# Kernel optimization log

Hardware: AMD Instinct MI355X
Metric: run time of the kernel (lower is better)

Reference implementation:

```python
import jax, jax.numpy as jnp
import numpy as np

N, E, H, R = 20000, 400000, 128, 20


def setup_inputs() -> dict:
    key = jax.random.key(0)
    ks = jax.random.split(key, 12)
    inv_h = 1.0 / np.sqrt(H)
    inv_r = 1.0 / np.sqrt(R)
    return {
        "s": jax.random.normal(ks[0], (N, H), jnp.float32),
        "v": jax.random.normal(ks[1], (N, 3, H), jnp.float32),
        "edge_rbf": jax.random.normal(ks[2], (E, R), jnp.float32),
        "edge_cutoff": jax.random.uniform(ks[3], (E,), jnp.float32),
        "edge_vec": jax.random.normal(ks[4], (E, 3), jnp.float32),
        "W1": jax.random.normal(ks[5], (H, H), jnp.float32) * inv_h,
        "b1": jnp.zeros((H,), jnp.float32),
        "W2": jax.random.normal(ks[6], (H, 3 * H), jnp.float32) * inv_h,
        "b2": jnp.zeros((3 * H,), jnp.float32),
        "Wr": jax.random.normal(ks[7], (R, 3 * H), jnp.float32) * inv_r,
        "br": jnp.zeros((3 * H,), jnp.float32),
        "edge_index": jax.random.randint(ks[8], (2, E), 0, N, jnp.int64),
    }


def reference(s, v, edge_rbf, edge_cutoff, edge_vec, W1, b1, W2, b2, Wr, br, edge_index):
    i, j = edge_index[0], edge_index[1]
    n = s.shape[0]
    # rbf projection modulated by cutoff: [E, 3H]
    W = (edge_rbf @ Wr + br) * edge_cutoff[:, None]
    # scalar MLP on gathered source features: [E, 3H]
    h = jax.nn.silu(s[j] @ W1 + b1)
    x = (h @ W2 + b2) * W
    x_ss, x_sv, x_vv = jnp.split(x, 3, axis=-1)  # each [E, H]
    ds = jax.ops.segment_sum(x_ss, i, num_segments=n)
    # dv1: outer product of edge direction with gated scalars -> [E,3,H]
    dv1 = jax.ops.segment_sum(x_sv[:, None, :] * edge_vec[:, :, None], i, num_segments=n)
    # equivariant term: project v_j onto edge direction, re-expand
    inner = jnp.sum(v[j] * edge_vec[:, :, None], axis=1)  # [E, H]
    dv2 = jax.ops.segment_sum((inner * x_vv)[:, None, :] * edge_vec[:, :, None], i, num_segments=n)
    return ds, dv1 + dv2
```

## Files before the change

kernel.cpp:

```cpp
#include <hip/hip_runtime.h>
#include <hip/hip_bf16.h>

#define HDIM 128
#define H3   384
#define RDIM 20
#define NPB  16
#define NPR  4
#define CHNK 16

typedef unsigned short u16;
typedef unsigned int   u32;
typedef __attribute__((ext_vector_type(8))) short short8v;
typedef __attribute__((ext_vector_type(4))) float f32x4;

__device__ __forceinline__ u16 f2bf(float f) {
    __hip_bfloat16 h = __float2bfloat16(f);
    return *(u16*)&h;
}
__device__ __forceinline__ float bf2f(u16 u) {
    union { u32 i; float f; } x; x.i = (u32)u << 16; return x.f;
}
__device__ __forceinline__ float bflo(u32 u) {
    union { u32 i; float f; } x; x.i = u << 16; return x.f;
}
__device__ __forceinline__ float bfhi(u32 u) {
    union { u32 i; float f; } x; x.i = u & 0xffff0000u; return x.f;
}
__device__ __forceinline__ u32 pk(float lo, float hi) {
    return (u32)f2bf(lo) | ((u32)f2bf(hi) << 16);
}

__global__ __launch_bounds__(128) void node_mlp_kernel(
    const float* __restrict__ s, const float* __restrict__ W1,
    const float* __restrict__ b1, const float* __restrict__ W2,
    const float* __restrict__ b2, const float* __restrict__ v,
    u32* __restrict__ PA, u32* __restrict__ PB, u32* __restrict__ PC, int N)
{
    __shared__ float sS[NPB][HDIM];
    __shared__ float sH[NPB][HDIM];
    const int t  = threadIdx.x;
    const int n0 = blockIdx.x * NPB;

    #pragma unroll
    for (int n = 0; n < NPB; ++n) {
        int node = n0 + n;
        sS[n][t] = (node < N) ? s[(size_t)node * HDIM + t] : 0.f;
    }
    __syncthreads();

    float acc[NPB];
    #pragma unroll
    for (int n = 0; n < NPB; ++n) acc[n] = 0.f;
    for (int k = 0; k < HDIM; ++k) {
        float w = W1[k * HDIM + t];
        #pragma unroll
        for (int n = 0; n < NPB; ++n) acc[n] += sS[n][k] * w;
    }
    float bb = b1[t];
    #pragma unroll
    for (int n = 0; n < NPB; ++n) {
        float z = acc[n] + bb;
        sH[n][t] = z / (1.f + __expf(-z));
    }
    __syncthreads();

    float a0[NPB], a1[NPB], a2[NPB];
    #pragma unroll
    for (int n = 0; n < NPB; ++n) { a0[n] = 0.f; a1[n] = 0.f; a2[n] = 0.f; }
    for (int k2 = 0; k2 < HDIM / 2; ++k2) {
        float2 hv[NPB];
        #pragma unroll
        for (int n = 0; n < NPB; ++n) hv[n] = ((const float2*)sH[n])[k2];
        #pragma unroll
        for (int kk = 0; kk < 2; ++kk) {
            int k = 2 * k2 + kk;
            float w0 = W2[k * H3 + t];
            float w1 = W2[k * H3 + t + 128];
            float w2 = W2[k * H3 + t + 256];
            #pragma unroll
            for (int n = 0; n < NPB; ++n) {
                float h = kk ? hv[n].y : hv[n].x;
                a0[n] += h * w0;
                a1[n] += h * w1;
                a2[n] += h * w2;
            }
        }
    }
    float c0 = b2[t], c1 = b2[t + 128], c2 = b2[t + 256];
    #pragma unroll
    for (int n = 0; n < NPB; ++n) {
        int node = n0 + n;
        if (node < N) {
            size_t vb = (size_t)node * H3;
            float vx = v[vb + t], vy = v[vb + 128 + t], vz = v[vb + 256 + t];
            size_t pb = (size_t)node * HDIM + t;
            PA[pb] = pk(a0[n] + c0, a1[n] + c1);
            PB[pb] = pk(a2[n] + c2, vx);
            PC[pb] = pk(vy, vz);
        }
    }
}

__global__ void hist_kernel(const int* __restrict__ eidx, int* __restrict__ counts, int E)
{
    int e = blockIdx.x * 256 + threadIdx.x;
    if (e < E) atomicAdd(&counts[eidx[e]], 1);
}

__global__ __launch_bounds__(1024) void scan_kernel(
    const int* __restrict__ counts, int* __restrict__ rstart,
    int* __restrict__ cursor, int N)
{
    __shared__ int part[1024];
    const int t = threadIdx.x;
    const int C = 20;
    int loc[C];
    int s = 0;
    #pragma unroll
    for (int q = 0; q < C; ++q) {
        int idx = t * C + q;
        int c = (idx < N) ? counts[idx] : 0;
        loc[q] = s; s += c;
    }
    part[t] = s;
    __syncthreads();
    for (int off = 1; off < 1024; off <<= 1) {
        int vv = (t >= off) ? part[t - off] : 0;
        __syncthreads();
        part[t] += vv;
        __syncthreads();
    }
    int boff = (t > 0) ? part[t - 1] : 0;
    #pragma unroll
    for (int q = 0; q < C; ++q) {
        int idx = t * C + q;
        if (idx < N) {
            int st = boff + loc[q];
            rstart[idx] = st;
            cursor[idx] = st;
        }
    }
    if (t == 1023) rstart[N] = part[1023];
}

__global__ void scatter_kernel(const int* __restrict__ eidx, int* __restrict__ cursor,
                               int* __restrict__ eord, int E)
{
    int e = blockIdx.x * 256 + threadIdx.x;
    if (e < E) {
        int i = eidx[e];
        int pos = atomicAdd(&cursor[i], 1);
        eord[pos] = e;
    }
}

__global__ __launch_bounds__(128) void reduce_kernel(
    const int* __restrict__ rstart, const int* __restrict__ eord,
    const float* __restrict__ rbf, const float* __restrict__ cutoff,
    const float* __restrict__ evec, const float* __restrict__ Wr,
    const float* __restrict__ br, const u32* __restrict__ PA,
    const u32* __restrict__ PB, const u32* __restrict__ PC,
    const int* __restrict__ eidx, float* __restrict__ ds,
    float* __restrict__ dv, int E, int N)
{
    const int t    = threadIdx.x;
    const int lane = t & 63;
    const int wave = t >> 6;
    const int g    = lane >> 4;
    const int m    = lane & 15;

    short8v bfrag[12];
    #pragma unroll
    for (int n = 0; n < 12; ++n) {
        int col = wave * 192 + n * 16 + m;
        short8v f;
        #pragma unroll
        for (int j = 0; j < 8; ++j) {
            int k = 8 * g + j;
            float val = (k < RDIM) ? Wr[k * H3 + col] : 0.f;
            f[j] = (short)f2bf(val);
        }
        bfrag[n] = f;
    }
    float br0 = br[t], br1 = br[t + 128], br2 = br[t + 256];

    __shared__ int   sE[CHNK], sJ[CHNK];
    __shared__ float sCut[CHNK], sVx[CHNK], sVy[CHNK], sVz[CHNK];
    __shared__ u16   Wl[CHNK][H3];

    for (int nn = 0; nn < NPR; ++nn) {
        int node = blockIdx.x * NPR + nn;
        if (node >= N) break;
        int beg = rstart[node], end = rstart[node + 1];
        float accs = 0.f, accx = 0.f, accy = 0.f, accz = 0.f;

        for (int c0 = beg; c0 < end; c0 += CHNK) {
            int cnt = min(CHNK, end - c0);
            __syncthreads();
            if (t < CHNK) {
                int e = eord[c0 + ((t < cnt) ? t : 0)];
                sE[t]   = e;
                sJ[t]   = eidx[E + e];
                sCut[t] = cutoff[e];
                sVx[t]  = evec[3 * e];
                sVy[t]  = evec[3 * e + 1];
                sVz[t]  = evec[3 * e + 2];
            }
            __syncthreads();

            short8v af;
            if (g == 3) {
                #pragma unroll
                for (int j = 0; j < 8; ++j) af[j] = 0;
            } else {
                const float* rrow = rbf + (size_t)sE[m] * RDIM;
                if (g < 2) {
                    float4 r0 = *(const float4*)(rrow + 8 * g);
                    float4 r1 = *(const float4*)(rrow + 8 * g + 4);
                    af[0] = (short)f2bf(r0.x); af[1] = (short)f2bf(r0.y);
                    af[2] = (short)f2bf(r0.z); af[3] = (short)f2bf(r0.w);
                    af[4] = (short)f2bf(r1.x); af[5] = (short)f2bf(r1.y);
                    af[6] = (short)f2bf(r1.z); af[7] = (short)f2bf(r1.w);
                } else {
                    float4 r0 = *(const float4*)(rrow + 16);
                    af[0] = (short)f2bf(r0.x); af[1] = (short)f2bf(r0.y);
                    af[2] = (short)f2bf(r0.z); af[3] = (short)f2bf(r0.w);
                    af[4] = 0; af[5] = 0; af[6] = 0; af[7] = 0;
                }
            }

            #pragma unroll
            for (int n = 0; n < 12; ++n) {
                f32x4 c = {0.f, 0.f, 0.f, 0.f};
                c = __builtin_amdgcn_mfma_f32_16x16x32_bf16(af, bfrag[n], c, 0, 0, 0);
                int col = wave * 192 + n * 16 + m;
                #pragma unroll
                for (int r = 0; r < 4; ++r)
                    Wl[4 * g + r][col] = f2bf(c[r]);
            }
            __syncthreads();

            u32 ca, cb, cc;
            {
                size_t pj = (size_t)sJ[0] * HDIM + t;
                ca = PA[pj]; cb = PB[pj]; cc = PC[pj];
            }
            for (int q = 0; q < cnt; ++q) {
                u32 na = 0, nb = 0, nc = 0;
                if (q + 1 < cnt) {
                    size_t pj = (size_t)sJ[q + 1] * HDIM + t;
                    na = PA[pj]; nb = PB[pj]; nc = PC[pj];
                }
                float w0 = bf2f(Wl[q][t]);
                float w1 = bf2f(Wl[q][t + 128]);
                float w2 = bf2f(Wl[q][t + 256]);
                float cu = sCut[q];
                float ex = sVx[q], ey = sVy[q], ez = sVz[q];
                float pss = bflo(ca), psv = bfhi(ca);
                float pvv = bflo(cb), vx  = bfhi(cb);
                float vy  = bflo(cc), vz  = bfhi(cc);
                float xss = (w0 + br0) * cu * pss;
                float xsv = (w1 + br1) * cu * psv;
                float xvv = (w2 + br2) * cu * pvv;
                float inner = vx * ex + vy * ey + vz * ez;
                float coef  = xsv + inner * xvv;
                accs += xss;
                accx += coef * ex;
                accy += coef * ey;
                accz += coef * ez;
                ca = na; cb = nb; cc = nc;
            }
        }

        ds[(size_t)node * HDIM + t] = accs;
        size_t dvi = (size_t)node * H3;
        dv[dvi + t]       = accx;
        dv[dvi + 128 + t] = accy;
        dv[dvi + 256 + t] = accz;
    }
}

extern "C" void kernel_launch(void* const* d_in, const int* in_sizes, int n_in,
                              void* d_out, int out_size, void* d_ws, size_t ws_size,
                              hipStream_t stream)
{
    const float* s    = (const float*)d_in[0];
    const float* v    = (const float*)d_in[1];
    const float* rbf  = (const float*)d_in[2];
    const float* cut  = (const float*)d_in[3];
    const float* evec = (const float*)d_in[4];
    const float* W1   = (const float*)d_in[5];
    const float* b1   = (const float*)d_in[6];
    const float* W2   = (const float*)d_in[7];
    const float* b2   = (const float*)d_in[8];
    const float* Wr   = (const float*)d_in[9];
    const float* br   = (const float*)d_in[10];
    const int*   eidx = (const int*)d_in[11];

    const int N = in_sizes[0] / HDIM;
    const int E = in_sizes[3];

    float* out = (float*)d_out;
    float* ds  = out;
    float* dv  = out + (size_t)N * HDIM;

    char* w = (char*)d_ws;
    u32* PA = (u32*)w;                     w += ((size_t)N * HDIM * 4 + 255) / 256 * 256;
    u32* PB = (u32*)w;                     w += ((size_t)N * HDIM * 4 + 255) / 256 * 256;
    u32* PC = (u32*)w;                     w += ((size_t)N * HDIM * 4 + 255) / 256 * 256;
    int* counts = (int*)w;                 w += ((size_t)N * 4 + 255) / 256 * 256;
    int* rstart = (int*)w;                 w += ((size_t)(N + 1) * 4 + 255) / 256 * 256;
    int* cursor = (int*)w;                 w += ((size_t)N * 4 + 255) / 256 * 256;
    int* eord   = (int*)w;

    hipMemsetAsync(counts, 0, (size_t)N * sizeof(int), stream);

    node_mlp_kernel<<<(N + NPB - 1) / NPB, 128, 0, stream>>>(s, W1, b1, W2, b2, v,
                                                             PA, PB, PC, N);
    hist_kernel<<<(E + 255) / 256, 256, 0, stream>>>(eidx, counts, E);
    scan_kernel<<<1, 1024, 0, stream>>>(counts, rstart, cursor, N);
    scatter_kernel<<<(E + 255) / 256, 256, 0, stream>>>(eidx, cursor, eord, E);
    reduce_kernel<<<(N + NPR - 1) / NPR, 128, 0, stream>>>(rstart, eord, rbf, cut, evec,
                                                           Wr, br, PA, PB, PC, eidx,
                                                           ds, dv, E, N);
}
```

Measured before the change: 369.3 us.

## Split edge loop across four thread groups, replace MFMA rbf projection with FP32 FMAs

```diff
diff --git a/kernel.cpp b/kernel.cpp
--- a/kernel.cpp
+++ b/kernel.cpp
@@ -6,19 +6,15 @@
 #define RDIM 20
 #define NPB  16
 #define NPR  4
-#define CHNK 16
+#define CHNK 32
+#define RBLK 512
 
 typedef unsigned short u16;
 typedef unsigned int   u32;
-typedef __attribute__((ext_vector_type(8))) short short8v;
-typedef __attribute__((ext_vector_type(4))) float f32x4;
 
 __device__ __forceinline__ u16 f2bf(float f) {
     __hip_bfloat16 h = __float2bfloat16(f);
     return *(u16*)&h;
-}
-__device__ __forceinline__ float bf2f(u16 u) {
-    union { u32 i; float f; } x; x.i = (u32)u << 16; return x.f;
 }
 __device__ __forceinline__ float bflo(u32 u) {
     union { u32 i; float f; } x; x.i = u << 16; return x.f;
@@ -34,7 +30,7 @@
     const float* __restrict__ s, const float* __restrict__ W1,
     const float* __restrict__ b1, const float* __restrict__ W2,
     const float* __restrict__ b2, const float* __restrict__ v,
-    u32* __restrict__ PA, u32* __restrict__ PB, u32* __restrict__ PC, int N)
+    u32* __restrict__ P3, int N)
 {
     __shared__ float sS[NPB][HDIM];
     __shared__ float sH[NPB][HDIM];
@@ -93,10 +89,10 @@
         if (node < N) {
             size_t vb = (size_t)node * H3;
             float vx = v[vb + t], vy = v[vb + 128 + t], vz = v[vb + 256 + t];
-            size_t pb = (size_t)node * HDIM + t;
-            PA[pb] = pk(a0[n] + c0, a1[n] + c1);
-            PB[pb] = pk(a2[n] + c2, vx);
-            PC[pb] = pk(vy, vz);
+            size_t pb = (size_t)node * H3 + t;
+            P3[pb]       = pk(a0[n] + c0, a1[n] + c1);
+            P3[pb + 128] = pk(a2[n] + c2, vx);
+            P3[pb + 256] = pk(vy, vz);
         }
     }
 }
@@ -154,39 +150,31 @@
     }
 }
 
-__global__ __launch_bounds__(128) void reduce_kernel(
+__global__ __launch_bounds__(RBLK) void reduce_kernel(
     const int* __restrict__ rstart, const int* __restrict__ eord,
     const float* __restrict__ rbf, const float* __restrict__ cutoff,
     const float* __restrict__ evec, const float* __restrict__ Wr,
-    const float* __restrict__ br, const u32* __restrict__ PA,
-    const u32* __restrict__ PB, const u32* __restrict__ PC,
+    const float* __restrict__ br, const u32* __restrict__ P3,
     const int* __restrict__ eidx, float* __restrict__ ds,
     float* __restrict__ dv, int E, int N)
 {
-    const int t    = threadIdx.x;
-    const int lane = t & 63;
-    const int wave = t >> 6;
-    const int g    = lane >> 4;
-    const int m    = lane & 15;
-
-    short8v bfrag[12];
-    #pragma unroll
-    for (int n = 0; n < 12; ++n) {
-        int col = wave * 192 + n * 16 + m;
-        short8v f;
-        #pragma unroll
-        for (int j = 0; j < 8; ++j) {
-            int k = 8 * g + j;
-            float val = (k < RDIM) ? Wr[k * H3 + col] : 0.f;
-            f[j] = (short)f2bf(val);
-        }
-        bfrag[n] = f;
-    }
-    float br0 = br[t], br1 = br[t + 128], br2 = br[t + 256];
-
-    __shared__ int   sE[CHNK], sJ[CHNK];
+    const int t  = threadIdx.x;
+    const int ch = t & (HDIM - 1);
+    const int u  = t >> 7;
+
+    float wr0[RDIM], wr1[RDIM], wr2[RDIM];
+    #pragma unroll
+    for (int k = 0; k < RDIM; ++k) {
+        wr0[k] = Wr[k * H3 + ch];
+        wr1[k] = Wr[k * H3 + ch + 128];
+        wr2[k] = Wr[k * H3 + ch + 256];
+    }
+    const float br0 = br[ch], br1 = br[ch + 128], br2 = br[ch + 256];
+
+    __shared__ int   sJoff[CHNK];
     __shared__ float sCut[CHNK], sVx[CHNK], sVy[CHNK], sVz[CHNK];
-    __shared__ u16   Wl[CHNK][H3];
+    __shared__ __attribute__((aligned(16))) float sRbf[CHNK][RDIM];
+    __shared__ float sRed[3][4][HDIM];
 
     for (int nn = 0; nn < NPR; ++nn) {
         int node = blockIdx.x * NPR + nn;
@@ -197,63 +185,43 @@
         for (int c0 = beg; c0 < end; c0 += CHNK) {
             int cnt = min(CHNK, end - c0);
             __syncthreads();
-            if (t < CHNK) {
-                int e = eord[c0 + ((t < cnt) ? t : 0)];
-                sE[t]   = e;
-                sJ[t]   = eidx[E + e];
-                sCut[t] = cutoff[e];
-                sVx[t]  = evec[3 * e];
-                sVy[t]  = evec[3 * e + 1];
-                sVz[t]  = evec[3 * e + 2];
+            if (t < cnt) {
+                int e = eord[c0 + t];
+                sJoff[t] = eidx[E + e] * H3;
+                sCut[t]  = cutoff[e];
+                sVx[t]   = evec[3 * e];
+                sVy[t]   = evec[3 * e + 1];
+                sVz[t]   = evec[3 * e + 2];
+            }
+            for (int x = t; x < cnt * RDIM; x += RBLK) {
+                int n = x / RDIM, k = x - n * RDIM;
+                int e = eord[c0 + n];
+                sRbf[n][k] = rbf[(size_t)e * RDIM + k];
             }
             __syncthreads();
 
-            short8v af;
-            if (g == 3) {
+            int q = u;
+            u32 ca = 0, cb = 0, cc = 0;
+            if (q < cnt) {
+                int idx = sJoff[q] + ch;
+                ca = P3[idx]; cb = P3[idx + 128]; cc = P3[idx + 256];
+            }
+            for (; q < cnt; q += 4) {
+                int qn = q + 4;
+                u32 na = 0, nb = 0, nc = 0;
+                if (qn < cnt) {
+                    int idx = sJoff[qn] + ch;
+                    na = P3[idx]; nb = P3[idx + 128]; nc = P3[idx + 256];
+                }
+                const float4* r4 = (const float4*)sRbf[q];
+                float w0 = 0.f, w1 = 0.f, w2 = 0.f;
                 #pragma unroll
-                for (int j = 0; j < 8; ++j) af[j] = 0;
-            } else {
-                const float* rrow = rbf + (size_t)sE[m] * RDIM;
-                if (g < 2) {
-                    float4 r0 = *(const float4*)(rrow + 8 * g);
-                    float4 r1 = *(const float4*)(rrow + 8 * g + 4);
-                    af[0] = (short)f2bf(r0.x); af[1] = (short)f2bf(r0.y);
-                    af[2] = (short)f2bf(r0.z); af[3] = (short)f2bf(r0.w);
-                    af[4] = (short)f2bf(r1.x); af[5] = (short)f2bf(r1.y);
-                    af[6] = (short)f2bf(r1.z); af[7] = (short)f2bf(r1.w);
-                } else {
-                    float4 r0 = *(const float4*)(rrow + 16);
-                    af[0] = (short)f2bf(r0.x); af[1] = (short)f2bf(r0.y);
-                    af[2] = (short)f2bf(r0.z); af[3] = (short)f2bf(r0.w);
-                    af[4] = 0; af[5] = 0; af[6] = 0; af[7] = 0;
+                for (int k4 = 0; k4 < 5; ++k4) {
+                    float4 r = r4[k4];
+                    w0 += r.x * wr0[4*k4] + r.y * wr0[4*k4+1] + r.z * wr0[4*k4+2] + r.w * wr0[4*k4+3];
+                    w1 += r.x * wr1[4*k4] + r.y * wr1[4*k4+1] + r.z * wr1[4*k4+2] + r.w * wr1[4*k4+3];
+                    w2 += r.x * wr2[4*k4] + r.y * wr2[4*k4+1] + r.z * wr2[4*k4+2] + r.w * wr2[4*k4+3];
                 }
-            }
-
-            #pragma unroll
-            for (int n = 0; n < 12; ++n) {
-                f32x4 c = {0.f, 0.f, 0.f, 0.f};
-                c = __builtin_amdgcn_mfma_f32_16x16x32_bf16(af, bfrag[n], c, 0, 0, 0);
-                int col = wave * 192 + n * 16 + m;
-                #pragma unroll
-                for (int r = 0; r < 4; ++r)
-                    Wl[4 * g + r][col] = f2bf(c[r]);
-            }
-            __syncthreads();
-
-            u32 ca, cb, cc;
-            {
-                size_t pj = (size_t)sJ[0] * HDIM + t;
-                ca = PA[pj]; cb = PB[pj]; cc = PC[pj];
-            }
-            for (int q = 0; q < cnt; ++q) {
-                u32 na = 0, nb = 0, nc = 0;
-                if (q + 1 < cnt) {
-                    size_t pj = (size_t)sJ[q + 1] * HDIM + t;
-                    na = PA[pj]; nb = PB[pj]; nc = PC[pj];
-                }
-                float w0 = bf2f(Wl[q][t]);
-                float w1 = bf2f(Wl[q][t + 128]);
-                float w2 = bf2f(Wl[q][t + 256]);
                 float cu = sCut[q];
                 float ex = sVx[q], ey = sVy[q], ez = sVz[q];
                 float pss = bflo(ca), psv = bfhi(ca);
@@ -272,11 +240,25 @@
             }
         }
 
-        ds[(size_t)node * HDIM + t] = accs;
-        size_t dvi = (size_t)node * H3;
-        dv[dvi + t]       = accx;
-        dv[dvi + 128 + t] = accy;
-        dv[dvi + 256 + t] = accz;
+        __syncthreads();
+        if (u > 0) {
+            sRed[u - 1][0][ch] = accs;
+            sRed[u - 1][1][ch] = accx;
+            sRed[u - 1][2][ch] = accy;
+            sRed[u - 1][3][ch] = accz;
+        }
+        __syncthreads();
+        if (u == 0) {
+            accs += sRed[0][0][ch] + sRed[1][0][ch] + sRed[2][0][ch];
+            accx += sRed[0][1][ch] + sRed[1][1][ch] + sRed[2][1][ch];
+            accy += sRed[0][2][ch] + sRed[1][2][ch] + sRed[2][2][ch];
+            accz += sRed[0][3][ch] + sRed[1][3][ch] + sRed[2][3][ch];
+            ds[(size_t)node * HDIM + ch] = accs;
+            size_t dvi = (size_t)node * H3;
+            dv[dvi + ch]       = accx;
+            dv[dvi + 128 + ch] = accy;
+            dv[dvi + 256 + ch] = accz;
+        }
     }
 }
 
@@ -305,9 +287,7 @@
     float* dv  = out + (size_t)N * HDIM;
 
     char* w = (char*)d_ws;
-    u32* PA = (u32*)w;                     w += ((size_t)N * HDIM * 4 + 255) / 256 * 256;
-    u32* PB = (u32*)w;                     w += ((size_t)N * HDIM * 4 + 255) / 256 * 256;
-    u32* PC = (u32*)w;                     w += ((size_t)N * HDIM * 4 + 255) / 256 * 256;
+    u32* P3 = (u32*)w;                     w += ((size_t)N * H3 * 4 + 255) / 256 * 256;
     int* counts = (int*)w;                 w += ((size_t)N * 4 + 255) / 256 * 256;
     int* rstart = (int*)w;                 w += ((size_t)(N + 1) * 4 + 255) / 256 * 256;
     int* cursor = (int*)w;                 w += ((size_t)N * 4 + 255) / 256 * 256;
@@ -315,12 +295,10 @@
 
     hipMemsetAsync(counts, 0, (size_t)N * sizeof(int), stream);
 
-    node_mlp_kernel<<<(N + NPB - 1) / NPB, 128, 0, stream>>>(s, W1, b1, W2, b2, v,
-                                                             PA, PB, PC, N);
+    node_mlp_kernel<<<(N + NPB - 1) / NPB, 128, 0, stream>>>(s, W1, b1, W2, b2, v, P3, N);
     hist_kernel<<<(E + 255) / 256, 256, 0, stream>>>(eidx, counts, E);
     scan_kernel<<<1, 1024, 0, stream>>>(counts, rstart, cursor, N);
     scatter_kernel<<<(E + 255) / 256, 256, 0, stream>>>(eidx, cursor, eord, E);
-    reduce_kernel<<<(N + NPR - 1) / NPR, 128, 0, stream>>>(rstart, eord, rbf, cut, evec,
-                                                           Wr, br, PA, PB, PC, eidx,
-                                                           ds, dv, E, N);
-}
+    reduce_kernel<<<(N + NPR - 1) / NPR, RBLK, 0, stream>>>(rstart, eord, rbf, cut, evec,
+                                                            Wr, br, P3, eidx, ds, dv, E, N);
+}
```

Result: faster. 346.7 us (-6.1%).
